# Performance work log

Measured on AMD Instinct MI355X. Metric: run time of the kernel, lower is better.

## Reference

```python
import jax, jax.numpy as jnp
import numpy as np

B, S, HID = 1, 2048, 4096
H = 32
Q_LORA, KV_LORA = 1536, 512
NOPE, ROPE, VDIM = 128, 64, 128
EPS = 1e-6
ROPE_BASE = 10000.0


def rms_norm(x, w, eps=EPS):
    var = jnp.mean(x.astype(jnp.float32) ** 2, axis=-1, keepdims=True)
    return (x * jax.lax.rsqrt(var + eps)).astype(x.dtype) * w


def rope_cos_sin(position_ids, dim=ROPE):
    inv_freq = 1.0 / (ROPE_BASE ** (jnp.arange(0, dim, 2, dtype=jnp.float32) / dim))
    ang = position_ids.astype(jnp.float32)[..., None] * inv_freq  # [B,S,dim/2]
    return jnp.cos(ang), jnp.sin(ang)


def apply_rope(x, cos, sin):
    # x: [..., dim]; neox-style rotate_half on the rope slice
    d2 = x.shape[-1] // 2
    x1, x2 = x[..., :d2], x[..., d2:]
    return jnp.concatenate([x1 * cos - x2 * sin, x2 * cos + x1 * sin], axis=-1)


def setup_inputs() -> dict:
    key = jax.random.key(0)
    ks = jax.random.split(key, 8)
    s = 0.02
    return {
        "position_ids": jnp.broadcast_to(jnp.arange(S, dtype=jnp.int32), (B, S)),
        "hidden_states": jax.random.normal(ks[0], (B, S, HID), jnp.float32),
        "w_fused_a": jax.random.normal(ks[1], (Q_LORA + KV_LORA + ROPE, HID), jnp.float32) * s,
        "q_a_ln_w": jnp.ones((Q_LORA,), jnp.float32),
        "kv_a_ln_w": jnp.ones((KV_LORA,), jnp.float32),
        "w_q_b": jax.random.normal(ks[2], (H * (NOPE + ROPE), Q_LORA), jnp.float32) * s,
        "w_kv_b": jax.random.normal(ks[3], (H * 2 * NOPE, KV_LORA), jnp.float32) * s,
        "w_o": jax.random.normal(ks[4], (HID, H * VDIM), jnp.float32) * s,
    }


def reference(position_ids, hidden_states, w_fused_a, q_a_ln_w, kv_a_ln_w, w_q_b, w_kv_b, w_o):
    # fused A projection: -> [q_lora | kv_lora | rope]
    a = jnp.einsum('bsh,oh->bso', hidden_states, w_fused_a)
    cq = rms_norm(a[..., :Q_LORA], q_a_ln_w)
    ckv = rms_norm(a[..., Q_LORA:Q_LORA + KV_LORA], kv_a_ln_w)
    k_pe = a[..., Q_LORA + KV_LORA:]  # [B,S,ROPE], shared across heads

    # Q up-projection, split nope/rope per head
    q = jnp.einsum('bsr,or->bso', cq, w_q_b).reshape(B, S, H, NOPE + ROPE)
    q_nope, q_pe = q[..., :NOPE], q[..., NOPE:]

    # KV up-projection: per head [k_nope | v]
    kv = jnp.einsum('bsr,or->bso', ckv, w_kv_b).reshape(B, S, H, 2 * NOPE)
    k_nope, v = kv[..., :NOPE], kv[..., NOPE:]

    # RoPE on the rope slices only
    cos, sin = rope_cos_sin(position_ids)  # [B,S,ROPE/2]
    q_pe = apply_rope(q_pe, cos[:, :, None, :], sin[:, :, None, :])
    k_pe = apply_rope(k_pe, cos, sin)

    qf = jnp.concatenate([q_nope, q_pe], axis=-1)  # [B,S,H,NOPE+ROPE]
    kf = jnp.concatenate([k_nope, jnp.broadcast_to(k_pe[:, :, None, :], (B, S, H, ROPE))], axis=-1)

    scale = 1.0 / np.sqrt(NOPE + ROPE)
    scores = jnp.einsum('bshd,bthd->bhst', qf, kf) * scale
    causal = jnp.tril(jnp.ones((S, S), dtype=bool))
    scores = jnp.where(causal, scores, jnp.finfo(scores.dtype).min)
    p = jax.nn.softmax(scores, axis=-1)
    attn = jnp.einsum('bhst,bthd->bshd', p, v).reshape(B, S, H * VDIM)
    return jnp.einsum('bsd,od->bso', attn, w_o)
```

## Files before the change

kernel.cpp:

```cpp
#include <hip/hip_runtime.h>
#include <cmath>

#define S_LEN 2048
#define HID 4096
#define NHEAD 32
#define Q_LORA 1536
#define KV_LORA 512
#define NOPE 128
#define ROPE_D 64
#define VDIM 128
#define QK_DIM 192
#define FUSED_N 2112
#define FUSED_NPAD 2304

typedef __attribute__((ext_vector_type(8))) short short8;
typedef __attribute__((ext_vector_type(4))) short short4v;
typedef __attribute__((ext_vector_type(4))) float floatx4;
typedef unsigned short ushort_t;

__device__ inline short f2bf(float f) {
    union { float f; unsigned u; } v; v.f = f;
    unsigned r = (v.u + 0x7fffu + ((v.u >> 16) & 1u)) >> 16;
    return (short)r;
}
__device__ inline float bf2f(ushort_t u) {
    union { unsigned u; float f; } v; v.u = ((unsigned)u) << 16; return v.f;
}

#define GLOAD16(g, l)                                                        \
    __builtin_amdgcn_global_load_lds(                                        \
        (const __attribute__((address_space(1))) unsigned int*)(g),          \
        (__attribute__((address_space(3))) unsigned int*)(l), 16, 0, 0)

__device__ inline short8 conv8(const float* s) {
    const float4* s4 = (const float4*)s;
    float4 a = s4[0], b = s4[1];
    short8 v;
    v[0] = f2bf(a.x); v[1] = f2bf(a.y); v[2] = f2bf(a.z); v[3] = f2bf(a.w);
    v[4] = f2bf(b.x); v[5] = f2bf(b.y); v[6] = f2bf(b.z); v[7] = f2bf(b.w);
    return v;
}

#define CE0 (S_LEN * HID)
#define CE1 (CE0 + FUSED_NPAD * HID)
#define CE2 (CE1 + NHEAD * QK_DIM * Q_LORA)
#define CE3 (CE2 + NHEAD * 256 * KV_LORA)

__global__ __launch_bounds__(256) void conv_all(
    const float* __restrict__ hs, const float* __restrict__ w_a,
    const float* __restrict__ w_qb, const float* __restrict__ w_kvb,
    ushort_t* __restrict__ hs_bf, ushort_t* __restrict__ w_a_bf,
    ushort_t* __restrict__ w_qb_bf, ushort_t* __restrict__ w_kvb_bf)
{
    int i = (blockIdx.x * 256 + threadIdx.x) * 8;
    if (i < CE0) {
        *(short8*)(hs_bf + i) = conv8(hs + i);
    } else if (i < CE1) {
        int j = i - CE0;
        short8 v;
        if (j < FUSED_N * HID) v = conv8(w_a + j);
        else                   v = (short8){0,0,0,0,0,0,0,0};
        *(short8*)(w_a_bf + j) = v;
    } else if (i < CE2) {
        int j = i - CE1;
        *(short8*)(w_qb_bf + j) = conv8(w_qb + j);
    } else if (i < CE3) {
        int j = i - CE2;
        *(short8*)(w_kvb_bf + j) = conv8(w_kvb + j);
    }
}

__global__ __launch_bounds__(256) void conv_bf16(
    const float* __restrict__ src, ushort_t* __restrict__ dst, int n)
{
    int i = (blockIdx.x * 256 + threadIdx.x) * 8;
    if (i >= n) return;
    *(short8*)(dst + i) = conv8(src + i);
}

__global__ __launch_bounds__(256) void reduce_add_f32(
    const float* __restrict__ p0, const float* __restrict__ p1,
    float* __restrict__ o, int n)
{
    int i = (blockIdx.x * 256 + threadIdx.x) * 4;
    if (i >= n) return;
    float4 a = *(const float4*)(p0 + i);
    float4 b = *(const float4*)(p1 + i);
    float4 c; c.x = a.x + b.x; c.y = a.y + b.y; c.z = a.z + b.z; c.w = a.w + b.w;
    *(float4*)(o + i) = c;
}

__device__ __forceinline__ void gemm_pipe_body(
    const ushort_t* __restrict__ A, int lda,
    const ushort_t* __restrict__ B, int ldb,
    int m0, int n0, int kbeg, int nst,
    short8* LDS, floatx4 (&acc)[8][4], int tid)
{
    const int lane = tid & 63;
    const int wave = tid >> 6;
    const int m    = lane & 15;
    const int quad = lane >> 4;
    const int wr   = wave >> 2;
    const int wc   = wave & 3;

    auto stage = [&](int k0, int buf) {
        short8* dst = &LDS[buf * 2048];
        #pragma unroll
        for (int r = 0; r < 2; ++r) {
            int i  = tid + r * 512;
            int mi = i & 15, qd = (i >> 4) & 3, rb = i >> 6;
            GLOAD16(A + (size_t)(m0 + rb * 16 + mi) * lda + k0 + qd * 8, dst + i);
            GLOAD16(B + (size_t)(n0 + rb * 16 + mi) * ldb + k0 + qd * 8, dst + 1024 + i);
        }
    };

    stage(kbeg, 0);
    stage(kbeg + 32, 1);

    for (int i = 0; i < nst; ++i) {
        if (i + 2 < nst) {
            stage(kbeg + (i + 2) * 32, (i + 2) & 3);
            asm volatile("s_waitcnt vmcnt(8)" ::: "memory");
        } else if (i + 1 < nst) {
            asm volatile("s_waitcnt vmcnt(4)" ::: "memory");
        } else {
            asm volatile("s_waitcnt vmcnt(0)" ::: "memory");
        }
        asm volatile("s_barrier" ::: "memory");

        const short8* As = &LDS[(i & 3) * 2048];
        const short8* Bs = As + 1024;
        short8 af[8], bfr[4];
        #pragma unroll
        for (int ii = 0; ii < 8; ++ii)
            af[ii] = As[((wr * 8 + ii) * 4 + quad) * 16 + m];
        #pragma unroll
        for (int j = 0; j < 4; ++j)
            bfr[j] = Bs[((wc * 4 + j) * 4 + quad) * 16 + m];

        __builtin_amdgcn_s_setprio(1);
        #pragma unroll
        for (int ri = 0; ri < 8; ++ri)
            #pragma unroll
            for (int ci = 0; ci < 4; ++ci)
                acc[ri][ci] = __builtin_amdgcn_mfma_f32_16x16x32_bf16(
                    af[ri], bfr[ci], acc[ri][ci], 0, 0, 0);
        __builtin_amdgcn_s_setprio(0);
    }
}

__device__ inline void store_c(float* p, float v)    { *p = v; }
__device__ inline void store_c(ushort_t* p, float v) { *p = (ushort_t)f2bf(v); }

template <typename CT>
__device__ __forceinline__ void gemm256_store(
    CT* __restrict__ C, int ldc, int N, int m0, int n0,
    floatx4 (&acc)[8][4], int tid)
{
    const int lane = tid & 63;
    const int wave = tid >> 6;
    const int m    = lane & 15;
    const int quad = lane >> 4;
    const int wr   = wave >> 2, wc = wave & 3;
    #pragma unroll
    for (int ci = 0; ci < 4; ++ci) {
        int col = n0 + wc * 64 + ci * 16 + m;
        if (col < N) {
            #pragma unroll
            for (int ri = 0; ri < 8; ++ri) {
                int row = m0 + wr * 128 + ri * 16 + quad * 4;
                #pragma unroll
                for (int r = 0; r < 4; ++r)
                    store_c(&C[(size_t)(row + r) * ldc + col], acc[ri][ci][r]);
            }
        }
    }
}

template <typename CT>
__global__ __launch_bounds__(512) void gemm256p(
    const ushort_t* __restrict__ A, int lda,
    const ushort_t* __restrict__ B, int ldb,
    CT* __restrict__ C, int ldc, int N, int Klen, int nx, int ny)
{
    __shared__ short8 LDS[4 * 2048];
    const int tid = threadIdx.x;

    const int nwg = gridDim.x;
    const int bid = blockIdx.x;
    const int wg  = (bid & 7) * (nwg >> 3) + (bid >> 3);
    const int nxy = nx * ny;
    const int z   = wg / nxy;
    const int rxy = wg - z * nxy;
    const int m0  = (rxy / nx) * 256;
    const int n0  = (rxy % nx) * 256;
    CT* Cz = C + (size_t)z * (size_t)ny * 256 * ldc;

    floatx4 acc[8][4];
    #pragma unroll
    for (int i = 0; i < 8; ++i)
        #pragma unroll
        for (int j = 0; j < 4; ++j) acc[i][j] = (floatx4){0.f, 0.f, 0.f, 0.f};

    gemm_pipe_body(A, lda, B, ldb, m0, n0, z * Klen, Klen >> 5, LDS, acc, tid);
    gemm256_store<CT>(Cz, ldc, N, m0, n0, acc, tid);
}

__global__ __launch_bounds__(512) void gemm34p(
    const ushort_t* __restrict__ a_bf,
    const ushort_t* __restrict__ w_qb_bf,
    const ushort_t* __restrict__ w_kvb_bf,
    ushort_t* __restrict__ q_bf,
    ushort_t* __restrict__ kv_bf,
    ushort_t* __restrict__ vt)
{
    __shared__ short8 LDS[4 * 2048];
    const int tid = threadIdx.x;

    const int nwg = gridDim.x;
    const int bid = blockIdx.x;
    const int wg  = (bid & 7) * (nwg >> 3) + (bid >> 3);
    const int x   = wg % 56;
    const int m0  = (wg / 56) * 256;

    const ushort_t* A; const ushort_t* B;
    int ldb, K, n0;
    if (x < 24) {
        A = a_bf;            B = w_qb_bf;
        ldb = Q_LORA;        K = Q_LORA;   n0 = x * 256;
    } else {
        A = a_bf + Q_LORA;   B = w_kvb_bf;
        ldb = KV_LORA;       K = KV_LORA;  n0 = (x - 24) * 256;
    }

    floatx4 acc[8][4];
    #pragma unroll
    for (int i = 0; i < 8; ++i)
        #pragma unroll
        for (int j = 0; j < 4; ++j) acc[i][j] = (floatx4){0.f, 0.f, 0.f, 0.f};

    gemm_pipe_body(A, FUSED_N, B, ldb, m0, n0, 0, K >> 5, LDS, acc, tid);

    const int lane = tid & 63;
    const int wave = tid >> 6;
    const int m    = lane & 15;
    const int quad = lane >> 4;
    const int wr   = wave >> 2, wc = wave & 3;

    if (x < 24) {
        gemm256_store<ushort_t>(q_bf, NHEAD * QK_DIM, NHEAD * QK_DIM, m0, n0, acc, tid);
    } else {
        const int h = x - 24;
        #pragma unroll
        for (int ci = 0; ci < 4; ++ci) {
            int dd = wc * 64 + ci * 16 + m;
            if (dd < 128) {
                #pragma unroll
                for (int ri = 0; ri < 8; ++ri) {
                    int row = m0 + wr * 128 + ri * 16 + quad * 4;
                    #pragma unroll
                    for (int r = 0; r < 4; ++r)
                        kv_bf[(size_t)(row + r) * (NHEAD * 256) + h * 256 + dd] =
                            (ushort_t)f2bf(acc[ri][ci][r]);
                }
            } else {
                int d = dd - 128;
                #pragma unroll
                for (int ri = 0; ri < 8; ++ri) {
                    int row0 = m0 + wr * 128 + ri * 16 + quad * 4;
                    short4v v4;
                    #pragma unroll
                    for (int r = 0; r < 4; ++r) v4[r] = f2bf(acc[ri][ci][r]);
                    *(short4v*)(vt + (((size_t)h * (S_LEN / 8) + (row0 >> 3)) * 128 + d) * 8
                                   + (row0 & 7)) = v4;
                }
            }
        }
    }
}

__global__ __launch_bounds__(256) void norm_rope_kernel(
    const float* __restrict__ part,
    ushort_t* __restrict__ a,
    const float* __restrict__ q_ln_w,
    const float* __restrict__ kv_ln_w,
    const int* __restrict__ pos_ids)
{
    const int s = blockIdx.x;
    const size_t PL = (size_t)S_LEN * FUSED_N;
    const float* r0 = part + (size_t)s * FUSED_N;
    ushort_t* row = a + (size_t)s * FUSED_N;
    __shared__ float red[256];
    const int tid = threadIdx.x;

    float vq[6];
    float ss = 0.f;
    #pragma unroll
    for (int j = 0; j < 6; ++j) {
        int i = tid + j * 256;
        vq[j] = (r0[i] + r0[i + PL]) + (r0[i + 2 * PL] + r0[i + 3 * PL]);
        ss += vq[j] * vq[j];
    }
    red[tid] = ss;
    __syncthreads();
    for (int w = 128; w > 0; w >>= 1) {
        if (tid < w) red[tid] += red[tid + w];
        __syncthreads();
    }
    float scale_q = rsqrtf(red[0] / (float)Q_LORA + 1e-6f);
    #pragma unroll
    for (int j = 0; j < 6; ++j) {
        int i = tid + j * 256;
        row[i] = (ushort_t)f2bf(vq[j] * scale_q * q_ln_w[i]);
    }
    __syncthreads();

    float vk[2];
    ss = 0.f;
    #pragma unroll
    for (int j = 0; j < 2; ++j) {
        int iw = tid + j * 256;
        int i  = Q_LORA + iw;
        vk[j] = (r0[i] + r0[i + PL]) + (r0[i + 2 * PL] + r0[i + 3 * PL]);
        ss += vk[j] * vk[j];
    }
    red[tid] = ss;
    __syncthreads();
    for (int w = 128; w > 0; w >>= 1) {
        if (tid < w) red[tid] += red[tid + w];
        __syncthreads();
    }
    float scale_kv = rsqrtf(red[0] / (float)KV_LORA + 1e-6f);
    #pragma unroll
    for (int j = 0; j < 2; ++j) {
        int iw = tid + j * 256;
        row[Q_LORA + iw] = (ushort_t)f2bf(vk[j] * scale_kv * kv_ln_w[iw]);
    }

    if (tid < 32) {
        const int j = tid;
        float pos = (float)pos_ids[s];
        float inv_freq = expf(-(float)j * (9.210340371976184f / 32.f));
        float ang = pos * inv_freq;
        float c = cosf(ang), sn = sinf(ang);
        int i1 = Q_LORA + KV_LORA + j;
        int i2 = i1 + 32;
        float x1 = (r0[i1] + r0[i1 + PL]) + (r0[i1 + 2 * PL] + r0[i1 + 3 * PL]);
        float x2 = (r0[i2] + r0[i2 + PL]) + (r0[i2 + 2 * PL] + r0[i2 + 3 * PL]);
        row[i1] = (ushort_t)f2bf(x1 * c - x2 * sn);
        row[i2] = (ushort_t)f2bf(x2 * c + x1 * sn);
    }
}

__global__ __launch_bounds__(256) void rope_q_kernel(
    ushort_t* __restrict__ q, const int* __restrict__ pos_ids)
{
    int idx = blockIdx.x * blockDim.x + threadIdx.x;
    if (idx >= S_LEN * NHEAD) return;
    int s = idx >> 5;
    float pos = (float)pos_ids[s];
    ushort_t* qp = q + (size_t)idx * QK_DIM + NOPE;
    #pragma unroll 4
    for (int j = 0; j < 32; ++j) {
        float inv_freq = expf(-(float)j * (9.210340371976184f / 32.f));
        float ang = pos * inv_freq;
        float c = cosf(ang), sn = sinf(ang);
        float x1 = bf2f(qp[j]), x2 = bf2f(qp[32 + j]);
        qp[j]      = (ushort_t)f2bf(x1 * c - x2 * sn);
        qp[32 + j] = (ushort_t)f2bf(x2 * c + x1 * sn);
    }
}

__global__ __launch_bounds__(256) void attn_mfma(
    const ushort_t* __restrict__ q,
    const ushort_t* __restrict__ kv,
    const ushort_t* __restrict__ abuf,
    const ushort_t* __restrict__ vt,
    ushort_t* __restrict__ attn)
{
    __shared__ short8 KF[3][768];
    __shared__ short8 VF[3][512];
    __shared__ short8 PA[256];

    const int tid  = threadIdx.x;
    const int wave = tid >> 6;
    const int lane = tid & 63;
    const int m    = lane & 15;
    const int quad = lane >> 4;
    const int h    = blockIdx.y;
    const int pair = blockIdx.x;
    const int qtiles[2] = { 31 - pair, pair };

    const float scale2 = 0.07216878364870323f * 1.4426950408889634f;
    short* pas = (short*)PA;

    auto stage_kv = [&](int t0, int buf) {
        #pragma unroll
        for (int rep = 0; rep < 3; ++rep) {
            int i   = rep * 256 + tid;
            int key = i & 31, qd = (i >> 5) & 3, c = i >> 7;
            if (c < 4)
                GLOAD16(kv + ((size_t)(t0 + key) * NHEAD + h) * 256 + c * 32 + qd * 8,
                        &KF[buf][i]);
            else
                GLOAD16(abuf + (size_t)(t0 + key) * FUSED_N + 2048 + (c - 4) * 32 + qd * 8,
                        &KF[buf][i]);
        }
        const ushort_t* vsrc = vt + ((size_t)h * (S_LEN / 8) + (t0 >> 3)) * 1024;
        GLOAD16(vsrc + (size_t)tid * 8, &VF[buf][tid]);
        GLOAD16(vsrc + (size_t)(256 + tid) * 8, &VF[buf][256 + tid]);
    };

    for (int qi = 0; qi < 2; ++qi) {
        const int q0 = qtiles[qi] * 64;
        const int qrow_base = q0 + wave * 16;

        short8 qf[6];
        {
            const ushort_t* qrow = q + ((size_t)(qrow_base + m) * NHEAD + h) * QK_DIM;
            #pragma unroll
            for (int c = 0; c < 6; ++c)
                qf[c] = *(const short8*)(qrow + c * 32 + quad * 8);
        }

        floatx4 O[8];
        #pragma unroll
        for (int t = 0; t < 8; ++t) O[t] = (floatx4){0.f, 0.f, 0.f, 0.f};
        float mrow[4] = {-1e30f, -1e30f, -1e30f, -1e30f};
        float lrow[4] = {0.f, 0.f, 0.f, 0.f};

        const int ntile = (q0 + 64) / 32;

        stage_kv(0, 0);

        for (int tt = 0; tt < ntile; ++tt) {
            const int t0 = tt * 32;
            if (tt + 1 < ntile) {
                stage_kv(t0 + 32, (tt + 1) % 3);
                asm volatile("s_waitcnt vmcnt(5)" ::: "memory");
            } else {
                asm volatile("s_waitcnt vmcnt(0)" ::: "memory");
            }
            asm volatile("s_barrier" ::: "memory");
            const int cur = tt % 3;

            floatx4 s0 = (floatx4){0.f, 0.f, 0.f, 0.f};
            floatx4 s1 = (floatx4){0.f, 0.f, 0.f, 0.f};
            const int kb = quad * 32 + m;
            __builtin_amdgcn_s_setprio(1);
            #pragma unroll
            for (int c = 0; c < 6; ++c) {
                s0 = __builtin_amdgcn_mfma_f32_16x16x32_bf16(qf[c], KF[cur][c * 128 + kb],      s0, 0, 0, 0);
                s1 = __builtin_amdgcn_mfma_f32_16x16x32_bf16(qf[c], KF[cur][c * 128 + kb + 16], s1, 0, 0, 0);
            }
            __builtin_amdgcn_s_setprio(0);

            const int qb = qrow_base + quad * 4;
            float sv0[4], sv1[4];
            #pragma unroll
            for (int r = 0; r < 4; ++r) {
                float a0 = s0[r] * scale2;
                float a1 = s1[r] * scale2;
                if (t0 + m > qb + r)      a0 = -1e30f;
                if (t0 + 16 + m > qb + r) a1 = -1e30f;
                sv0[r] = a0; sv1[r] = a1;
            }
            #pragma unroll
            for (int r = 0; r < 4; ++r) {
                float v = fmaxf(sv0[r], sv1[r]);
                if (!__all(v <= mrow[r] + 8.f)) {
                    v = fmaxf(v, __shfl_xor(v, 1));
                    v = fmaxf(v, __shfl_xor(v, 2));
                    v = fmaxf(v, __shfl_xor(v, 4));
                    v = fmaxf(v, __shfl_xor(v, 8));
                    float mnew  = fmaxf(mrow[r], v);
                    float alpha = exp2f(mrow[r] - mnew);
                    lrow[r] *= alpha;
                    #pragma unroll
                    for (int t = 0; t < 8; ++t) O[t][r] *= alpha;
                    mrow[r] = mnew;
                }
                float p0 = exp2f(sv0[r] - mrow[r]);
                float p1 = exp2f(sv1[r] - mrow[r]);
                lrow[r] += p0 + p1;
                int row = quad * 4 + r;
                short* pw = pas + wave * 512;
                pw[((m >> 3) + 0) * 128 + row * 8 + (m & 7)] = f2bf(p0);
                pw[((m >> 3) + 2) * 128 + row * 8 + (m & 7)] = f2bf(p1);
            }

            short8 pfrag = PA[wave * 64 + quad * 16 + m];
            __builtin_amdgcn_s_setprio(1);
            #pragma unroll
            for (int t = 0; t < 8; ++t) {
                O[t] = __builtin_amdgcn_mfma_f32_16x16x32_bf16(
                    pfrag, VF[cur][quad * 128 + m + 16 * t], O[t], 0, 0, 0);
            }
            __builtin_amdgcn_s_setprio(0);
        }

        #pragma unroll
        for (int r = 0; r < 4; ++r) {
            float l = lrow[r];
            l += __shfl_xor(l, 1);
            l += __shfl_xor(l, 2);
            l += __shfl_xor(l, 4);
            l += __shfl_xor(l, 8);
            float linv = 1.f / l;
            int row = qrow_base + quad * 4 + r;
            ushort_t* dst = attn + ((size_t)row * NHEAD + h) * VDIM + m;
            #pragma unroll
            for (int t = 0; t < 8; ++t)
                dst[16 * t] = (ushort_t)f2bf(O[t][r] * linv);
        }
        asm volatile("s_barrier" ::: "memory");
    }
}

extern "C" void kernel_launch(void* const* d_in, const int* in_sizes, int n_in,
                              void* d_out, int out_size, void* d_ws, size_t ws_size,
                              hipStream_t stream)
{
    const int*   pos    = (const int*)d_in[0];
    const float* hs     = (const float*)d_in[1];
    const float* w_a    = (const float*)d_in[2];
    const float* qlnw   = (const float*)d_in[3];
    const float* kvlnw  = (const float*)d_in[4];
    const float* w_qb   = (const float*)d_in[5];
    const float* w_kvb  = (const float*)d_in[6];
    const float* w_o    = (const float*)d_in[7];
    float* out = (float*)d_out;

    char* p = (char*)d_ws;
    ushort_t* a_bf    = (ushort_t*)p; p += (size_t)S_LEN * FUSED_N * 2;
    ushort_t* q_bf    = (ushort_t*)p; p += (size_t)S_LEN * NHEAD * QK_DIM * 2;
    ushort_t* kv_bf   = (ushort_t*)p; p += (size_t)S_LEN * NHEAD * 256 * 2;
    ushort_t* attn_bf = (ushort_t*)p; p += (size_t)S_LEN * HID * 2;
    ushort_t* hs_bf   = (ushort_t*)p; p += (size_t)S_LEN * HID * 2;
    ushort_t* w_a_bf  = (ushort_t*)p; p += (size_t)FUSED_NPAD * HID * 2;
    ushort_t* w_qb_bf = (ushort_t*)p; p += (size_t)NHEAD * QK_DIM * Q_LORA * 2;
    ushort_t* w_kvb_bf= (ushort_t*)p; p += (size_t)NHEAD * 256 * KV_LORA * 2;
    ushort_t* vt_bf   = (ushort_t*)p; p += (size_t)S_LEN * HID * 2;
    ushort_t* w_o_bf  = hs_bf;
    float* part1 = (float*)q_bf;
    float* part7 = (float*)a_bf;

    if (ws_size < (size_t)(p - (char*)d_ws)) return;

    dim3 blk(256);
    dim3 blk512(512);
    auto cgrid = [](size_t n) { return dim3((unsigned)((n / 8 + 255) / 256)); };

    conv_all<<<dim3(CE3 / 2048), blk, 0, stream>>>(
        hs, w_a, w_qb, w_kvb, hs_bf, w_a_bf, w_qb_bf, w_kvb_bf);

    gemm256p<float><<<dim3((FUSED_NPAD / 256) * (S_LEN / 256) * 4), blk512, 0, stream>>>(
        hs_bf, HID, w_a_bf, HID, part1, FUSED_N, FUSED_N, HID / 4,
        FUSED_NPAD / 256, S_LEN / 256);

    conv_bf16<<<cgrid((size_t)HID * HID), blk, 0, stream>>>(w_o, w_o_bf, HID * HID);

    norm_rope_kernel<<<S_LEN, 256, 0, stream>>>(part1, a_bf, qlnw, kvlnw, pos);

    gemm34p<<<dim3(56 * (S_LEN / 256)), blk512, 0, stream>>>(
        a_bf, w_qb_bf, w_kvb_bf, q_bf, kv_bf, vt_bf);

    rope_q_kernel<<<(S_LEN * NHEAD + 255) / 256, 256, 0, stream>>>(q_bf, pos);

    attn_mfma<<<dim3(16, NHEAD), blk, 0, stream>>>(
        q_bf, kv_bf, a_bf, vt_bf, attn_bf);

    gemm256p<float><<<dim3((HID / 256) * (S_LEN / 256) * 2), blk512, 0, stream>>>(
        attn_bf, HID, w_o_bf, HID, part7, HID, HID, HID / 2,
        HID / 256, S_LEN / 256);
    reduce_add_f32<<<cgrid((size_t)S_LEN * HID * 2), blk, 0, stream>>>(
        part7, part7 + (size_t)S_LEN * HID, out, S_LEN * HID);
}
```

Measured before the change: 590.7 us.

## Fuse Q RoPE into attention and share KV tiles across paired query tiles

Removes the separate rope_q_kernel and applies the rotary embedding to the Q fragments in registers when the attention kernel loads them. The attention kernel also processes both paired query tiles in a single KV loop, so the shared prefix of K/V tiles is staged into LDS once instead of twice. This saves a kernel launch, a read-modify-write pass over Q, and redundant KV loads. In exchange it doubles the accumulator and Q registers per wave, which may lower occupancy or cause spills.

```diff
diff --git a/kernel.cpp b/kernel.cpp
--- a/kernel.cpp
+++ b/kernel.cpp
@@ -352,30 +352,67 @@
     }
 }
 
-__global__ __launch_bounds__(256) void rope_q_kernel(
-    ushort_t* __restrict__ q, const int* __restrict__ pos_ids)
-{
-    int idx = blockIdx.x * blockDim.x + threadIdx.x;
-    if (idx >= S_LEN * NHEAD) return;
-    int s = idx >> 5;
-    float pos = (float)pos_ids[s];
-    ushort_t* qp = q + (size_t)idx * QK_DIM + NOPE;
-    #pragma unroll 4
-    for (int j = 0; j < 32; ++j) {
-        float inv_freq = expf(-(float)j * (9.210340371976184f / 32.f));
-        float ang = pos * inv_freq;
-        float c = cosf(ang), sn = sinf(ang);
-        float x1 = bf2f(qp[j]), x2 = bf2f(qp[32 + j]);
-        qp[j]      = (ushort_t)f2bf(x1 * c - x2 * sn);
-        qp[32 + j] = (ushort_t)f2bf(x2 * c + x1 * sn);
-    }
-}
+#define ATTN_PROCESS(qf, O, mrow, lrow, qrb)                                   \
+    {                                                                          \
+        floatx4 s0 = (floatx4){0.f, 0.f, 0.f, 0.f};                            \
+        floatx4 s1 = (floatx4){0.f, 0.f, 0.f, 0.f};                            \
+        const int kb = quad * 32 + m;                                          \
+        __builtin_amdgcn_s_setprio(1);                                         \
+        _Pragma("unroll")                                                      \
+        for (int c = 0; c < 6; ++c) {                                          \
+            s0 = __builtin_amdgcn_mfma_f32_16x16x32_bf16(qf[c], KF[cur][c * 128 + kb],      s0, 0, 0, 0); \
+            s1 = __builtin_amdgcn_mfma_f32_16x16x32_bf16(qf[c], KF[cur][c * 128 + kb + 16], s1, 0, 0, 0); \
+        }                                                                      \
+        __builtin_amdgcn_s_setprio(0);                                         \
+        const int qb = (qrb) + quad * 4;                                       \
+        float sv0[4], sv1[4];                                                  \
+        _Pragma("unroll")                                                      \
+        for (int r = 0; r < 4; ++r) {                                          \
+            float a0 = s0[r] * scale2;                                         \
+            float a1 = s1[r] * scale2;                                         \
+            if (t0 + m > qb + r)      a0 = -1e30f;                             \
+            if (t0 + 16 + m > qb + r) a1 = -1e30f;                             \
+            sv0[r] = a0; sv1[r] = a1;                                          \
+        }                                                                      \
+        _Pragma("unroll")                                                      \
+        for (int r = 0; r < 4; ++r) {                                          \
+            float v = fmaxf(sv0[r], sv1[r]);                                   \
+            if (!__all(v <= mrow[r] + 8.f)) {                                  \
+                v = fmaxf(v, __shfl_xor(v, 1));                                \
+                v = fmaxf(v, __shfl_xor(v, 2));                                \
+                v = fmaxf(v, __shfl_xor(v, 4));                                \
+                v = fmaxf(v, __shfl_xor(v, 8));                                \
+                float mnew  = fmaxf(mrow[r], v);                               \
+                float alpha = exp2f(mrow[r] - mnew);                           \
+                lrow[r] *= alpha;                                              \
+                _Pragma("unroll")                                              \
+                for (int t = 0; t < 8; ++t) O[t][r] *= alpha;                  \
+                mrow[r] = mnew;                                                \
+            }                                                                  \
+            float p0 = exp2f(sv0[r] - mrow[r]);                                \
+            float p1 = exp2f(sv1[r] - mrow[r]);                                \
+            lrow[r] += p0 + p1;                                                \
+            int rw = quad * 4 + r;                                             \
+            short* pw = pas + wave * 512;                                      \
+            pw[((m >> 3) + 0) * 128 + rw * 8 + (m & 7)] = f2bf(p0);            \
+            pw[((m >> 3) + 2) * 128 + rw * 8 + (m & 7)] = f2bf(p1);            \
+        }                                                                      \
+        short8 pfrag = PA[wave * 64 + quad * 16 + m];                          \
+        __builtin_amdgcn_s_setprio(1);                                         \
+        _Pragma("unroll")                                                      \
+        for (int t = 0; t < 8; ++t) {                                          \
+            O[t] = __builtin_amdgcn_mfma_f32_16x16x32_bf16(                    \
+                pfrag, VF[cur][quad * 128 + m + 16 * t], O[t], 0, 0, 0);       \
+        }                                                                      \
+        __builtin_amdgcn_s_setprio(0);                                         \
+    }
 
 __global__ __launch_bounds__(256) void attn_mfma(
     const ushort_t* __restrict__ q,
     const ushort_t* __restrict__ kv,
     const ushort_t* __restrict__ abuf,
     const ushort_t* __restrict__ vt,
+    const int* __restrict__ pos_ids,
     ushort_t* __restrict__ attn)
 {
     __shared__ short8 KF[3][768];
@@ -389,7 +426,8 @@
     const int quad = lane >> 4;
     const int h    = blockIdx.y;
     const int pair = blockIdx.x;
-    const int qtiles[2] = { 31 - pair, pair };
+    const int qtA  = 31 - pair, qtB = pair;
+    const int ntA  = 2 * qtA + 2, ntB = 2 * qtB + 2;
 
     const float scale2 = 0.07216878364870323f * 1.4426950408889634f;
     short* pas = (short*)PA;
@@ -411,109 +449,91 @@
         GLOAD16(vsrc + (size_t)(256 + tid) * 8, &VF[buf][256 + tid]);
     };
 
-    for (int qi = 0; qi < 2; ++qi) {
-        const int q0 = qtiles[qi] * 64;
-        const int qrow_base = q0 + wave * 16;
-
-        short8 qf[6];
-        {
-            const ushort_t* qrow = q + ((size_t)(qrow_base + m) * NHEAD + h) * QK_DIM;
-            #pragma unroll
-            for (int c = 0; c < 6; ++c)
-                qf[c] = *(const short8*)(qrow + c * 32 + quad * 8);
-        }
-
-        floatx4 O[8];
-        #pragma unroll
-        for (int t = 0; t < 8; ++t) O[t] = (floatx4){0.f, 0.f, 0.f, 0.f};
-        float mrow[4] = {-1e30f, -1e30f, -1e30f, -1e30f};
-        float lrow[4] = {0.f, 0.f, 0.f, 0.f};
-
-        const int ntile = (q0 + 64) / 32;
-
-        stage_kv(0, 0);
-
-        for (int tt = 0; tt < ntile; ++tt) {
-            const int t0 = tt * 32;
-            if (tt + 1 < ntile) {
-                stage_kv(t0 + 32, (tt + 1) % 3);
-                asm volatile("s_waitcnt vmcnt(5)" ::: "memory");
-            } else {
-                asm volatile("s_waitcnt vmcnt(0)" ::: "memory");
-            }
-            asm volatile("s_barrier" ::: "memory");
-            const int cur = tt % 3;
-
-            floatx4 s0 = (floatx4){0.f, 0.f, 0.f, 0.f};
-            floatx4 s1 = (floatx4){0.f, 0.f, 0.f, 0.f};
-            const int kb = quad * 32 + m;
-            __builtin_amdgcn_s_setprio(1);
-            #pragma unroll
-            for (int c = 0; c < 6; ++c) {
-                s0 = __builtin_amdgcn_mfma_f32_16x16x32_bf16(qf[c], KF[cur][c * 128 + kb],      s0, 0, 0, 0);
-                s1 = __builtin_amdgcn_mfma_f32_16x16x32_bf16(qf[c], KF[cur][c * 128 + kb + 16], s1, 0, 0, 0);
-            }
-            __builtin_amdgcn_s_setprio(0);
-
-            const int qb = qrow_base + quad * 4;
-            float sv0[4], sv1[4];
-            #pragma unroll
-            for (int r = 0; r < 4; ++r) {
-                float a0 = s0[r] * scale2;
-                float a1 = s1[r] * scale2;
-                if (t0 + m > qb + r)      a0 = -1e30f;
-                if (t0 + 16 + m > qb + r) a1 = -1e30f;
-                sv0[r] = a0; sv1[r] = a1;
-            }
-            #pragma unroll
-            for (int r = 0; r < 4; ++r) {
-                float v = fmaxf(sv0[r], sv1[r]);
-                if (!__all(v <= mrow[r] + 8.f)) {
-                    v = fmaxf(v, __shfl_xor(v, 1));
-                    v = fmaxf(v, __shfl_xor(v, 2));
-                    v = fmaxf(v, __shfl_xor(v, 4));
-                    v = fmaxf(v, __shfl_xor(v, 8));
-                    float mnew  = fmaxf(mrow[r], v);
-                    float alpha = exp2f(mrow[r] - mnew);
-                    lrow[r] *= alpha;
-                    #pragma unroll
-                    for (int t = 0; t < 8; ++t) O[t][r] *= alpha;
-                    mrow[r] = mnew;
-                }
-                float p0 = exp2f(sv0[r] - mrow[r]);
-                float p1 = exp2f(sv1[r] - mrow[r]);
-                lrow[r] += p0 + p1;
-                int row = quad * 4 + r;
-                short* pw = pas + wave * 512;
-                pw[((m >> 3) + 0) * 128 + row * 8 + (m & 7)] = f2bf(p0);
-                pw[((m >> 3) + 2) * 128 + row * 8 + (m & 7)] = f2bf(p1);
-            }
-
-            short8 pfrag = PA[wave * 64 + quad * 16 + m];
-            __builtin_amdgcn_s_setprio(1);
-            #pragma unroll
-            for (int t = 0; t < 8; ++t) {
-                O[t] = __builtin_amdgcn_mfma_f32_16x16x32_bf16(
-                    pfrag, VF[cur][quad * 128 + m + 16 * t], O[t], 0, 0, 0);
-            }
-            __builtin_amdgcn_s_setprio(0);
-        }
-
-        #pragma unroll
-        for (int r = 0; r < 4; ++r) {
-            float l = lrow[r];
-            l += __shfl_xor(l, 1);
-            l += __shfl_xor(l, 2);
-            l += __shfl_xor(l, 4);
-            l += __shfl_xor(l, 8);
-            float linv = 1.f / l;
-            int row = qrow_base + quad * 4 + r;
-            ushort_t* dst = attn + ((size_t)row * NHEAD + h) * VDIM + m;
-            #pragma unroll
-            for (int t = 0; t < 8; ++t)
-                dst[16 * t] = (ushort_t)f2bf(O[t][r] * linv);
+    short8 qfA[6], qfB[6];
+    {
+        int rowA = qtA * 64 + wave * 16 + m;
+        int rowB = qtB * 64 + wave * 16 + m;
+        const ushort_t* qra = q + ((size_t)rowA * NHEAD + h) * QK_DIM;
+        const ushort_t* qrb = q + ((size_t)rowB * NHEAD + h) * QK_DIM;
+        #pragma unroll
+        for (int c = 0; c < 6; ++c) {
+            qfA[c] = *(const short8*)(qra + c * 32 + quad * 8);
+            qfB[c] = *(const short8*)(qrb + c * 32 + quad * 8);
+        }
+        float posA = (float)pos_ids[rowA];
+        float posB = (float)pos_ids[rowB];
+        #pragma unroll
+        for (int e = 0; e < 8; ++e) {
+            int j = quad * 8 + e;
+            float inv_freq = expf(-(float)j * (9.210340371976184f / 32.f));
+            float angA = posA * inv_freq, angB = posB * inv_freq;
+            float cA = cosf(angA), sA = sinf(angA);
+            float cB = cosf(angB), sB = sinf(angB);
+            float xa1 = bf2f((ushort_t)qfA[4][e]), xa2 = bf2f((ushort_t)qfA[5][e]);
+            float xb1 = bf2f((ushort_t)qfB[4][e]), xb2 = bf2f((ushort_t)qfB[5][e]);
+            qfA[4][e] = f2bf(xa1 * cA - xa2 * sA);
+            qfA[5][e] = f2bf(xa2 * cA + xa1 * sA);
+            qfB[4][e] = f2bf(xb1 * cB - xb2 * sB);
+            qfB[5][e] = f2bf(xb2 * cB + xb1 * sB);
+        }
+    }
+
+    floatx4 OA[8], OB[8];
+    #pragma unroll
+    for (int t = 0; t < 8; ++t) {
+        OA[t] = (floatx4){0.f, 0.f, 0.f, 0.f};
+        OB[t] = (floatx4){0.f, 0.f, 0.f, 0.f};
+    }
+    float mA[4] = {-1e30f, -1e30f, -1e30f, -1e30f};
+    float lA[4] = {0.f, 0.f, 0.f, 0.f};
+    float mB[4] = {-1e30f, -1e30f, -1e30f, -1e30f};
+    float lB[4] = {0.f, 0.f, 0.f, 0.f};
+
+    const int qrbA = qtA * 64 + wave * 16;
+    const int qrbB = qtB * 64 + wave * 16;
+
+    stage_kv(0, 0);
+
+    for (int tt = 0; tt < ntA; ++tt) {
+        const int t0 = tt * 32;
+        if (tt + 1 < ntA) {
+            stage_kv(t0 + 32, (tt + 1) % 3);
+            asm volatile("s_waitcnt vmcnt(5)" ::: "memory");
+        } else {
+            asm volatile("s_waitcnt vmcnt(0)" ::: "memory");
         }
         asm volatile("s_barrier" ::: "memory");
+        const int cur = tt % 3;
+
+        ATTN_PROCESS(qfA, OA, mA, lA, qrbA);
+        if (tt < ntB) ATTN_PROCESS(qfB, OB, mB, lB, qrbB);
+    }
+
+    #pragma unroll
+    for (int r = 0; r < 4; ++r) {
+        float la = lA[r];
+        la += __shfl_xor(la, 1);
+        la += __shfl_xor(la, 2);
+        la += __shfl_xor(la, 4);
+        la += __shfl_xor(la, 8);
+        float linvA = 1.f / la;
+        int rowA = qrbA + quad * 4 + r;
+        ushort_t* dstA = attn + ((size_t)rowA * NHEAD + h) * VDIM + m;
+        #pragma unroll
+        for (int t = 0; t < 8; ++t)
+            dstA[16 * t] = (ushort_t)f2bf(OA[t][r] * linvA);
+
+        float lb = lB[r];
+        lb += __shfl_xor(lb, 1);
+        lb += __shfl_xor(lb, 2);
+        lb += __shfl_xor(lb, 4);
+        lb += __shfl_xor(lb, 8);
+        float linvB = 1.f / lb;
+        int rowB = qrbB + quad * 4 + r;
+        ushort_t* dstB = attn + ((size_t)rowB * NHEAD + h) * VDIM + m;
+        #pragma unroll
+        for (int t = 0; t < 8; ++t)
+            dstB[16 * t] = (ushort_t)f2bf(OB[t][r] * linvB);
     }
 }
 
@@ -565,10 +585,8 @@
     gemm34p<<<dim3(56 * (S_LEN / 256)), blk512, 0, stream>>>(
         a_bf, w_qb_bf, w_kvb_bf, q_bf, kv_bf, vt_bf);
 
-    rope_q_kernel<<<(S_LEN * NHEAD + 255) / 256, 256, 0, stream>>>(q_bf, pos);
-
     attn_mfma<<<dim3(16, NHEAD), blk, 0, stream>>>(
-        q_bf, kv_bf, a_bf, vt_bf, attn_bf);
+        q_bf, kv_bf, a_bf, vt_bf, pos, attn_bf);
 
     gemm256p<float><<<dim3((HID / 256) * (S_LEN / 256) * 2), blk512, 0, stream>>>(
         attn_bf, HID, w_o_bf, HID, part7, HID, HID, HID / 2,
```

Measured after the change: 669.2 us. +13.3%, slower.
